# Optimization experiments

Hardware: AMD Instinct MI355X
Metric: run time of the kernel (lower is better)

The kernel has to match this reference:

```python
import jax, jax.numpy as jnp
import numpy as np

BETA = 0.25  # commitment-loss weight from init_kwargs

B, T, D, K = 16, 2048, 256, 1024


def setup_inputs() -> dict:
    key = jax.random.key(0)
    k1, k2 = jax.random.split(key)
    z_e = jax.random.normal(k1, (B, T, D), dtype=jnp.float32)
    codebook = jax.random.normal(k2, (K, D), dtype=jnp.float32)
    return {"z_e": z_e, "codebook": codebook}


def reference(z_e, codebook):
    # dot_z_embedding: tensordot over channel dim -> (B, T, K)
    dot = jnp.einsum("btd,kd->btk", z_e, codebook)
    norm_sq_z = jnp.sum(jnp.square(z_e), axis=-1, keepdims=True)      # (B, T, 1)
    norm_sq_e = jnp.sum(jnp.square(codebook), axis=-1)                # (K,)
    dist = -2.0 * dot + norm_sq_z + norm_sq_e                         # (B, T, K)
    ids = jnp.argmin(dist, axis=-1)                                   # (B, T) int
    z_q = codebook[ids]                                               # (B, T, D)
    # losses: tf.norm over the quantised axis, then mean
    loss_commit = jnp.mean(jnp.linalg.norm(jax.lax.stop_gradient(z_e) - z_q, axis=-1))
    loss_codebook = jnp.mean(jnp.linalg.norm(z_e - jax.lax.stop_gradient(z_q), axis=-1))
    loss_vq = loss_codebook + BETA * loss_commit
    similarity = dot / jnp.sqrt(norm_sq_z) / jnp.sqrt(norm_sq_e)      # (B, T, K) cosine
    return z_q, similarity, ids, loss_vq
```

## Files before the change

### kernel.cpp

```cpp
#include <hip/hip_runtime.h>


#define M_ROWS 32768
#define KCODES 1024
#define DDIM   256
#define ENC_BIG 33554432.0f

typedef __bf16 bf16_t;
typedef __attribute__((ext_vector_type(8))) bf16_t bf16x8;
typedef __attribute__((ext_vector_type(4))) float f32x4;

__device__ __forceinline__ unsigned f2bf(float f) {
  unsigned u = __float_as_uint(f);
  u += 0x7FFFu + ((u >> 16) & 1u);
  return u >> 16;
}

__device__ __forceinline__ float wave_sum(float p) {
#pragma unroll
  for (int o = 1; o < 64; o <<= 1) p += __shfl_xor(p, o);
  return p;
}
__device__ __forceinline__ float wave_min(float p) {
#pragma unroll
  for (int o = 1; o < 64; o <<= 1) p = fminf(p, __shfl_xor(p, o));
  return p;
}

__global__ __launch_bounds__(256) void prep_cb_kernel(
    const float* __restrict__ cb, unsigned short* __restrict__ cbb,
    float* __restrict__ nse, float* __restrict__ rsqe)
{
  const int t = threadIdx.x;
  const int lane = t & 63;
  const int r = blockIdx.x * 4 + (t >> 6);
  const float4 e = ((const float4*)cb)[(size_t)r * 64 + lane];
  ushort4 u;
  u.x = (unsigned short)f2bf(e.x); u.y = (unsigned short)f2bf(e.y);
  u.z = (unsigned short)f2bf(e.z); u.w = (unsigned short)f2bf(e.w);
  ((ushort4*)cbb)[(size_t)r * 64 + lane] = u;
  float p = wave_sum(e.x*e.x + e.y*e.y + e.z*e.z + e.w*e.w);
  if (lane == 0) { nse[r] = p; rsqe[r] = 1.0f / sqrtf(p); }
}

__global__ __launch_bounds__(256, 2) void gemm_kernel(
    const float* __restrict__ ze, const unsigned short* __restrict__ cbb,
    const float* __restrict__ rsqe_g, const float* __restrict__ nse_g,
    float* __restrict__ sim, float* __restrict__ cand)
{
  __shared__ __attribute__((aligned(128))) unsigned short A[128 * 64];
  __shared__ __attribute__((aligned(128))) unsigned short Bt[128 * 64];
  __shared__ float s_rsqz[128];

  const int t = threadIdx.x;
  const int wv = t >> 6, lane = t & 63;
  const int bid = blockIdx.x;
  const int swz = (bid & 7) * 256 + (bid >> 3);
  const long row0 = (long)(swz >> 3) * 128;
  const int  col0 = (swz & 7) * 128;

  f32x4 acc[4][4] = {};

  const int rr = lane >> 3, qq = lane & 7;
  const int sq = ((qq ^ rr) << 3);

  float nrm[4] = {0.f, 0.f, 0.f, 0.f};

  for (int kt = 0; kt < 4; ++kt) {
    const int k0 = kt * 64;
#pragma unroll
    for (int i = 0; i < 4; ++i) {
      const int rbase = wv * 32 + i * 8;
      const unsigned short* src = cbb + ((size_t)(col0 + rbase + rr)) * DDIM + k0 + sq;
      __builtin_amdgcn_global_load_lds((const __attribute__((address_space(1))) void*)src,
                                       (__attribute__((address_space(3))) void*)&Bt[rbase * 64],
                                       16, 0, 0);
    }
#pragma unroll
    for (int i = 0; i < 4; ++i) {
      const int idx = i * 256 + t;
      const int ar = idx >> 3, aq = idx & 7;
      const float4* p = (const float4*)(ze + (row0 + ar) * (size_t)DDIM + k0 + aq * 8);
      const float4 x = p[0], y = p[1];
      nrm[i] += x.x*x.x + x.y*x.y + x.z*x.z + x.w*x.w
              + y.x*y.x + y.y*y.y + y.z*y.z + y.w*y.w;
      uint4 u;
      u.x = f2bf(x.x) | (f2bf(x.y) << 16);
      u.y = f2bf(x.z) | (f2bf(x.w) << 16);
      u.z = f2bf(y.x) | (f2bf(y.y) << 16);
      u.w = f2bf(y.z) | (f2bf(y.w) << 16);
      *(uint4*)((char*)A + ar * 128 + ((aq ^ (ar & 7)) << 4)) = u;
    }
    __syncthreads();

    const int r16 = lane & 15, g = lane >> 4;
    const int wm = wv >> 1, wn = wv & 1;
#pragma unroll
    for (int ks = 0; ks < 2; ++ks) {
      bf16x8 af[4], bfr[4];
#pragma unroll
      for (int mi = 0; mi < 4; ++mi) {
        const int r = wm * 64 + mi * 16 + r16;
        const int ph = ((ks * 4 + g) ^ (r & 7)) << 4;
        af[mi] = *(const bf16x8*)((const char*)A + r * 128 + ph);
      }
#pragma unroll
      for (int ni = 0; ni < 4; ++ni) {
        const int r = wn * 64 + ni * 16 + r16;
        const int ph = ((ks * 4 + g) ^ (r & 7)) << 4;
        bfr[ni] = *(const bf16x8*)((const char*)Bt + r * 128 + ph);
      }
#pragma unroll
      for (int mi = 0; mi < 4; ++mi)
#pragma unroll
        for (int ni = 0; ni < 4; ++ni)
          acc[mi][ni] = __builtin_amdgcn_mfma_f32_16x16x32_bf16(af[mi], bfr[ni], acc[mi][ni], 0, 0, 0);
    }
    __syncthreads();
  }

#pragma unroll
  for (int i = 0; i < 4; ++i) {
    float p = nrm[i];
    p += __shfl_xor(p, 1); p += __shfl_xor(p, 2); p += __shfl_xor(p, 4);
    if ((t & 7) == 0) s_rsqz[(i * 256 + t) >> 3] = 1.0f / sqrtf(p);
  }
  __syncthreads();

  const int r16 = lane & 15, g = lane >> 4;
  const int wm = wv >> 1, wn = wv & 1;
  const int strip = (col0 >> 6) | wn;
#pragma unroll
  for (int mi = 0; mi < 4; ++mi) {
#pragma unroll
    for (int j = 0; j < 4; ++j) {
      const int rloc = wm * 64 + mi * 16 + g * 4 + j;
      const long row = row0 + rloc;
      const float rz = s_rsqz[rloc];
      float* so = sim + (size_t)row * KCODES + col0 + wn * 64 + r16;
      float e1 = ENC_BIG, e2 = ENC_BIG;
#pragma unroll
      for (int ni = 0; ni < 4; ++ni) {
        const int colk = col0 + wn * 64 + ni * 16 + r16;
        const float d = acc[mi][ni][j];
        so[ni * 16] = d * rz * rsqe_g[colk];
        const float v = nse_g[colk] - 2.0f * d;
        const float enc = floorf((v + 1024.0f) * 8.0f) * 1024.0f + (float)colk;
        if (enc < e1) { e2 = e1; e1 = enc; } else e2 = fminf(e2, enc);
      }
#pragma unroll
      for (int m = 1; m < 16; m <<= 1) {
        const float p1 = __shfl_xor(e1, m);
        const float p2 = __shfl_xor(e2, m);
        const float n1 = fminf(e1, p1);
        const float n2 = fminf(fmaxf(e1, p1), fminf(e2, p2));
        e1 = n1; e2 = n2;
      }
      if (r16 == 0)
        ((float2*)cand)[row * 16 + strip] = make_float2(e1, e2);
    }
  }
}

__global__ __launch_bounds__(256) void select1_kernel(
    const float* __restrict__ ze, const float* __restrict__ cb,
    const float* __restrict__ cand, const float* __restrict__ nse,
    float* __restrict__ ids)
{
  const int t = threadIdx.x;
  const int lane = t & 63;
  const int row  = blockIdx.x * 4 + (t >> 6);

  const float e = (lane < 32) ? cand[(size_t)row * 32 + lane] : ENC_BIG;
  const float m_enc = wave_min(e);
  const float qmin  = floorf(m_enc * 0.0009765625f);
  const float ql    = floorf(e * 0.0009765625f);
  unsigned long long msk = __ballot(ql <= qmin + 16.0f);
  int kbest;
  if (__popcll(msk) == 1) {
    kbest = ((int)m_enc) & 1023;
  } else {
    const float4 zr = ((const float4*)ze)[(size_t)row * 64 + lane];
    float tbest = INFINITY; kbest = KCODES;
    while (msk) {
      const int lb = __ffsll(msk) - 1;
      msk &= msk - 1;
      const int kc = ((int)__shfl(e, lb)) & 1023;
      const float4 er = ((const float4*)cb)[(size_t)kc * 64 + lane];
      const float p = wave_sum(zr.x*er.x + zr.y*er.y + zr.z*er.z + zr.w*er.w);
      const float tv = nse[kc] - 2.0f * p;
      if (tv < tbest || (tv == tbest && kc < kbest)) { tbest = tv; kbest = kc; }
    }
  }
  if (lane == 0) ids[row] = (float)kbest;
}

__global__ __launch_bounds__(256) void zq_loss_kernel(
    const float* __restrict__ ze, const float* __restrict__ cb,
    const float* __restrict__ ids,
    float* __restrict__ zq, float* __restrict__ partials)
{
  __shared__ float s_part[4];
  const int t = threadIdx.x;
  const int wv = t >> 6, lane = t & 63;
  const int row = blockIdx.x * 4 + wv;

  const int kbest = (int)ids[row];
  const float4 er = ((const float4*)cb)[(size_t)kbest * 64 + lane];
  const float4 zr = ((const float4*)ze)[(size_t)row * 64 + lane];
  ((float4*)zq)[(size_t)row * 64 + lane] = er;
  const float dx = zr.x - er.x, dy = zr.y - er.y, dz = zr.z - er.z, dw = zr.w - er.w;
  const float ss = wave_sum(dx*dx + dy*dy + dz*dz + dw*dw);
  if (lane == 0) s_part[wv] = sqrtf(ss);
  __syncthreads();
  if (t == 0)
    partials[blockIdx.x] = (s_part[0] + s_part[1]) + (s_part[2] + s_part[3]);
}

__global__ __launch_bounds__(256) void finalize_kernel(
    const float* __restrict__ partials, float* __restrict__ out_loss)
{
  __shared__ float s[4];
  const int t = threadIdx.x;
  float p = 0.0f;
#pragma unroll
  for (int i = 0; i < 32; ++i) p += partials[t + i * 256];
  p = wave_sum(p);
  if ((t & 63) == 0) s[t >> 6] = p;
  __syncthreads();
  if (t == 0) out_loss[0] = 1.25f * ((s[0] + s[1]) + (s[2] + s[3])) / 32768.0f;
}

extern "C" void kernel_launch(void* const* d_in, const int* in_sizes, int n_in,
                              void* d_out, int out_size, void* d_ws, size_t ws_size,
                              hipStream_t stream) {
  const float* ze = (const float*)d_in[0];
  const float* cb = (const float*)d_in[1];

  float* out  = (float*)d_out;
  float* zq   = out;
  float* sim  = out + 8388608;
  float* ids  = out + 41943040;
  float* lout = out + 41975808;

  float* cand = zq;

  char* w = (char*)d_ws;
  unsigned short* cbb = (unsigned short*)w;
  float* nse      = (float*)(w + 524288);
  float* rsqe     = (float*)(w + 528384);
  float* partials = (float*)(w + 532480);

  prep_cb_kernel<<<256, 256, 0, stream>>>(cb, cbb, nse, rsqe);
  gemm_kernel<<<2048, 256, 0, stream>>>(ze, cbb, rsqe, nse, sim, cand);
  select1_kernel<<<8192, 256, 0, stream>>>(ze, cb, cand, nse, ids);
  zq_loss_kernel<<<8192, 256, 0, stream>>>(ze, cb, ids, zq, partials);
  finalize_kernel<<<1, 256, 0, stream>>>(partials, lout);
}
```

Before: 90.25 us.

## Pre-convert z_e to bf16 in prep kernel and stream A tiles via global_load_lds

```diff
diff --git a/kernel.cpp b/kernel.cpp
--- a/kernel.cpp
+++ b/kernel.cpp
@@ -10,10 +10,10 @@
 typedef __attribute__((ext_vector_type(8))) bf16_t bf16x8;
 typedef __attribute__((ext_vector_type(4))) float f32x4;
 
-__device__ __forceinline__ unsigned f2bf(float f) {
+__device__ __forceinline__ unsigned short f2bf(float f) {
   unsigned u = __float_as_uint(f);
   u += 0x7FFFu + ((u >> 16) & 1u);
-  return u >> 16;
+  return (unsigned short)(u >> 16);
 }
 
 __device__ __forceinline__ float wave_sum(float p) {
@@ -27,35 +27,44 @@
   return p;
 }
 
-__global__ __launch_bounds__(256) void prep_cb_kernel(
-    const float* __restrict__ cb, unsigned short* __restrict__ cbb,
+__global__ __launch_bounds__(256) void prep_kernel(
+    const float* __restrict__ ze, const float* __restrict__ cb,
+    unsigned short* __restrict__ zb, unsigned short* __restrict__ cbb,
+    float* __restrict__ rsqz,
     float* __restrict__ nse, float* __restrict__ rsqe)
 {
   const int t = threadIdx.x;
   const int lane = t & 63;
-  const int r = blockIdx.x * 4 + (t >> 6);
-  const float4 e = ((const float4*)cb)[(size_t)r * 64 + lane];
-  ushort4 u;
-  u.x = (unsigned short)f2bf(e.x); u.y = (unsigned short)f2bf(e.y);
-  u.z = (unsigned short)f2bf(e.z); u.w = (unsigned short)f2bf(e.w);
-  ((ushort4*)cbb)[(size_t)r * 64 + lane] = u;
-  float p = wave_sum(e.x*e.x + e.y*e.y + e.z*e.z + e.w*e.w);
-  if (lane == 0) { nse[r] = p; rsqe[r] = 1.0f / sqrtf(p); }
+  const int row = blockIdx.x * 4 + (t >> 6);
+  if (row < M_ROWS) {
+    const float4 z = ((const float4*)ze)[(size_t)row * 64 + lane];
+    ushort4 u;
+    u.x = f2bf(z.x); u.y = f2bf(z.y); u.z = f2bf(z.z); u.w = f2bf(z.w);
+    ((ushort4*)zb)[(size_t)row * 64 + lane] = u;
+    float p = wave_sum(z.x*z.x + z.y*z.y + z.z*z.z + z.w*z.w);
+    if (lane == 0) rsqz[row] = 1.0f / sqrtf(p);
+  } else {
+    const int r = row - M_ROWS;
+    const float4 e = ((const float4*)cb)[(size_t)r * 64 + lane];
+    ushort4 u;
+    u.x = f2bf(e.x); u.y = f2bf(e.y); u.z = f2bf(e.z); u.w = f2bf(e.w);
+    ((ushort4*)cbb)[(size_t)r * 64 + lane] = u;
+    float p = wave_sum(e.x*e.x + e.y*e.y + e.z*e.z + e.w*e.w);
+    if (lane == 0) { nse[r] = p; rsqe[r] = 1.0f / sqrtf(p); }
+  }
 }
 
 __global__ __launch_bounds__(256, 2) void gemm_kernel(
-    const float* __restrict__ ze, const unsigned short* __restrict__ cbb,
-    const float* __restrict__ rsqe_g, const float* __restrict__ nse_g,
+    const unsigned short* __restrict__ zb, const unsigned short* __restrict__ cbb,
+    const float* __restrict__ rsqz, const float* __restrict__ rsqe_g,
+    const float* __restrict__ nse_g,
     float* __restrict__ sim, float* __restrict__ cand)
 {
-  __shared__ __attribute__((aligned(128))) unsigned short A[128 * 64];
-  __shared__ __attribute__((aligned(128))) unsigned short Bt[128 * 64];
-  __shared__ float s_rsqz[128];
-
-  const int t = threadIdx.x;
-  const int wv = t >> 6, lane = t & 63;
-  const int bid = blockIdx.x;
-  const int swz = (bid & 7) * 256 + (bid >> 3);
+  __shared__ __attribute__((aligned(128))) unsigned short lds[16384];
+  const int tid  = threadIdx.x;
+  const int wv   = tid >> 6, lane = tid & 63;
+  const int bid  = blockIdx.x;
+  const int swz  = (bid & 7) * 256 + (bid >> 3);
   const long row0 = (long)(swz >> 3) * 128;
   const int  col0 = (swz & 7) * 128;
 
@@ -64,51 +73,36 @@
   const int rr = lane >> 3, qq = lane & 7;
   const int sq = ((qq ^ rr) << 3);
 
-  float nrm[4] = {0.f, 0.f, 0.f, 0.f};
-
   for (int kt = 0; kt < 4; ++kt) {
     const int k0 = kt * 64;
 #pragma unroll
     for (int i = 0; i < 4; ++i) {
       const int rbase = wv * 32 + i * 8;
-      const unsigned short* src = cbb + ((size_t)(col0 + rbase + rr)) * DDIM + k0 + sq;
-      __builtin_amdgcn_global_load_lds((const __attribute__((address_space(1))) void*)src,
-                                       (__attribute__((address_space(3))) void*)&Bt[rbase * 64],
+      const unsigned short* srca = zb  + ((size_t)(row0 + rbase + rr)) * DDIM + k0 + sq;
+      const unsigned short* srcb = cbb + ((size_t)(col0 + rbase + rr)) * DDIM + k0 + sq;
+      __builtin_amdgcn_global_load_lds((const __attribute__((address_space(1))) void*)srca,
+                                       (__attribute__((address_space(3))) void*)&lds[rbase * 64],
                                        16, 0, 0);
-    }
-#pragma unroll
-    for (int i = 0; i < 4; ++i) {
-      const int idx = i * 256 + t;
-      const int ar = idx >> 3, aq = idx & 7;
-      const float4* p = (const float4*)(ze + (row0 + ar) * (size_t)DDIM + k0 + aq * 8);
-      const float4 x = p[0], y = p[1];
-      nrm[i] += x.x*x.x + x.y*x.y + x.z*x.z + x.w*x.w
-              + y.x*y.x + y.y*y.y + y.z*y.z + y.w*y.w;
-      uint4 u;
-      u.x = f2bf(x.x) | (f2bf(x.y) << 16);
-      u.y = f2bf(x.z) | (f2bf(x.w) << 16);
-      u.z = f2bf(y.x) | (f2bf(y.y) << 16);
-      u.w = f2bf(y.z) | (f2bf(y.w) << 16);
-      *(uint4*)((char*)A + ar * 128 + ((aq ^ (ar & 7)) << 4)) = u;
+      __builtin_amdgcn_global_load_lds((const __attribute__((address_space(1))) void*)srcb,
+                                       (__attribute__((address_space(3))) void*)&lds[8192 + rbase * 64],
+                                       16, 0, 0);
     }
     __syncthreads();
-
     const int r16 = lane & 15, g = lane >> 4;
-    const int wm = wv >> 1, wn = wv & 1;
 #pragma unroll
     for (int ks = 0; ks < 2; ++ks) {
       bf16x8 af[4], bfr[4];
 #pragma unroll
       for (int mi = 0; mi < 4; ++mi) {
-        const int r = wm * 64 + mi * 16 + r16;
-        const int ph = ((ks * 4 + g) ^ (r & 7)) << 4;
-        af[mi] = *(const bf16x8*)((const char*)A + r * 128 + ph);
+        const int r  = (wv >> 1) * 64 + mi * 16 + r16;
+        const int qy = ((ks * 4 + g) ^ (r & 7)) << 4;
+        af[mi] = *(const bf16x8*)((const char*)lds + r * 128 + qy);
       }
 #pragma unroll
       for (int ni = 0; ni < 4; ++ni) {
-        const int r = wn * 64 + ni * 16 + r16;
-        const int ph = ((ks * 4 + g) ^ (r & 7)) << 4;
-        bfr[ni] = *(const bf16x8*)((const char*)Bt + r * 128 + ph);
+        const int r  = (wv & 1) * 64 + ni * 16 + r16;
+        const int qy = ((ks * 4 + g) ^ (r & 7)) << 4;
+        bfr[ni] = *(const bf16x8*)((const char*)lds + 16384 + r * 128 + qy);
       }
 #pragma unroll
       for (int mi = 0; mi < 4; ++mi)
@@ -118,14 +112,6 @@
     }
     __syncthreads();
   }
-
-#pragma unroll
-  for (int i = 0; i < 4; ++i) {
-    float p = nrm[i];
-    p += __shfl_xor(p, 1); p += __shfl_xor(p, 2); p += __shfl_xor(p, 4);
-    if ((t & 7) == 0) s_rsqz[(i * 256 + t) >> 3] = 1.0f / sqrtf(p);
-  }
-  __syncthreads();
 
   const int r16 = lane & 15, g = lane >> 4;
   const int wm = wv >> 1, wn = wv & 1;
@@ -134,9 +120,8 @@
   for (int mi = 0; mi < 4; ++mi) {
 #pragma unroll
     for (int j = 0; j < 4; ++j) {
-      const int rloc = wm * 64 + mi * 16 + g * 4 + j;
-      const long row = row0 + rloc;
-      const float rz = s_rsqz[rloc];
+      const long row = row0 + wm * 64 + mi * 16 + g * 4 + j;
+      const float rz = rsqz[row];
       float* so = sim + (size_t)row * KCODES + col0 + wn * 64 + r16;
       float e1 = ENC_BIG, e2 = ENC_BIG;
 #pragma unroll
@@ -243,16 +228,18 @@
   float* ids  = out + 41943040;
   float* lout = out + 41975808;
 
-  float* cand = zq;
+  unsigned short* zb = (unsigned short*)d_out;
+  float* cand = (float*)((char*)d_out + 16777216);
 
   char* w = (char*)d_ws;
   unsigned short* cbb = (unsigned short*)w;
-  float* nse      = (float*)(w + 524288);
-  float* rsqe     = (float*)(w + 528384);
-  float* partials = (float*)(w + 532480);
-
-  prep_cb_kernel<<<256, 256, 0, stream>>>(cb, cbb, nse, rsqe);
-  gemm_kernel<<<2048, 256, 0, stream>>>(ze, cbb, rsqe, nse, sim, cand);
+  float* rsqz     = (float*)(w + 524288);
+  float* nse      = (float*)(w + 655360);
+  float* rsqe     = (float*)(w + 659456);
+  float* partials = (float*)(w + 663552);
+
+  prep_kernel<<<8448, 256, 0, stream>>>(ze, cb, zb, cbb, rsqz, nse, rsqe);
+  gemm_kernel<<<2048, 256, 0, stream>>>(zb, cbb, rsqz, rsqe, nse, sim, cand);
   select1_kernel<<<8192, 256, 0, stream>>>(ze, cb, cand, nse, ids);
   zq_loss_kernel<<<8192, 256, 0, stream>>>(ze, cb, ids, zq, partials);
   finalize_kernel<<<1, 256, 0, stream>>>(partials, lout);
```

Result: faster. 78.27 us (-13.3%).
